# Kernel optimization log

Measured on AMD Instinct MI355X. Metric: run time of the kernel, lower is better.

Reference implementation:

```python
import jax, jax.numpy as jnp
import numpy as np

NEG = -9e15
ALPHA = 0.2  # leaky_relu negative slope


def setup_inputs() -> dict:
    key = jax.random.key(0)
    k1, k2, k3, k4, k5 = jax.random.split(key, 5)
    N, F_in, F_out = 8192, 128, 128
    x = jax.random.normal(k1, (N, F_in), dtype=jnp.float32)
    adj = jax.random.randint(k2, (N, N), 0, 2).astype(jnp.float32)
    # xavier-ish scaled params
    W = jax.random.normal(k3, (F_in, F_out), dtype=jnp.float32) * (1.0 / np.sqrt(F_in))
    a1 = jax.random.normal(k4, (F_out,), dtype=jnp.float32) * (1.0 / np.sqrt(2 * F_out))
    a2 = jax.random.normal(k5, (F_out,), dtype=jnp.float32) * (1.0 / np.sqrt(2 * F_out))
    a_bias = jnp.zeros((1,), dtype=jnp.float32)
    return {"x": x, "adj": adj, "W": W, "a1": a1, "a2": a2, "a_bias": a_bias}


def reference(x, adj, W, a1, a2, a_bias):
    # h = W(input)                                   [N, F]
    h = x @ W
    # a(concat(h_i, h_j)) == h_i.a1 + h_j.a2 + b  -> avoids N*N*2F concat
    s1 = h @ a1  # [N]
    s2 = h @ a2  # [N]
    e = jax.nn.leaky_relu(s1[:, None] + s2[None, :] + a_bias[0], negative_slope=ALPHA)  # [N, N]
    e = jnp.where(adj > 0, e, NEG)
    attention = jax.nn.softmax(e, axis=1)
    # dropout p=0 (deterministic eval): identity
    return attention @ h
```

## Files before the change

kernel.cpp:

```cpp
#include <hip/hip_runtime.h>
#include <hip/hip_bf16.h>

typedef __attribute__((ext_vector_type(8)))  __bf16         bf16x8;
typedef __attribute__((ext_vector_type(4)))  float          f32x4;
typedef __attribute__((ext_vector_type(8)))  unsigned short u16x8;

#define LOG2E 1.44269504088896340736f

#if __has_builtin(__builtin_amdgcn_exp2f)
#define EXP2F(x) __builtin_amdgcn_exp2f(x)
#else
#define EXP2F(x) __builtin_exp2f(x)
#endif

__device__ __forceinline__ unsigned short f2b(float f) {
  union { __bf16 h; unsigned short s; } o; o.h = (__bf16)f; return o.s;
}

__global__ __launch_bounds__(256) void k_prep(
    const float* __restrict__ x, const float* __restrict__ W,
    const float* __restrict__ a1, const float* __restrict__ a2,
    const float* __restrict__ ab,
    unsigned short* __restrict__ hT, float* __restrict__ s1p,
    float* __restrict__ s2p) {
  __shared__ __align__(16) float Ws[64 * 128];
  __shared__ __align__(16) float Xs[16 * 128];
  const int t = threadIdx.x;
  const int rb = blockIdx.x * 16;
  const int r  = t >> 4;
  const int fg = t & 15;

  {
    int off = t * 8;
    *(f32x4*)(Xs + off)     = *(const f32x4*)(x + (long)rb * 128 + off);
    *(f32x4*)(Xs + off + 4) = *(const f32x4*)(x + (long)rb * 128 + off + 4);
  }

  float acc[8];
#pragma unroll
  for (int j = 0; j < 8; ++j) acc[j] = 0.f;

  for (int half = 0; half < 2; ++half) {
    __syncthreads();
#pragma unroll
    for (int c = 0; c < 8; ++c) {
      int off = c * 1024 + t * 4;
      *(f32x4*)(Ws + off) = *(const f32x4*)(W + half * 8192 + off);
    }
    __syncthreads();
    for (int k = 0; k < 64; ++k) {
      float xv = Xs[r * 128 + half * 64 + k];
      f32x4 w0 = *(const f32x4*)(Ws + k * 128 + fg * 8);
      f32x4 w1 = *(const f32x4*)(Ws + k * 128 + fg * 8 + 4);
#pragma unroll
      for (int j = 0; j < 4; ++j) {
        acc[j]     += xv * w0[j];
        acc[4 + j] += xv * w1[j];
      }
    }
  }

  float p1 = 0.f, p2 = 0.f;
#pragma unroll
  for (int j = 0; j < 8; ++j) {
    p1 += acc[j] * a1[fg * 8 + j];
    p2 += acc[j] * a2[fg * 8 + j];
  }
#pragma unroll
  for (int mask = 1; mask <= 8; mask <<= 1) {
    p1 += __shfl_xor(p1, mask, 64);
    p2 += __shfl_xor(p2, mask, 64);
  }
  if (fg == 0) {
    s1p[rb + r] = LOG2E * (p1 + ab[0]);
    s2p[rb + r] = LOG2E * p2;
  }
#pragma unroll
  for (int j = 0; j < 8; ++j)
    hT[(long)(fg * 8 + j) * 8192 + rb + r] = f2b(acc[j]);
}

__global__ __launch_bounds__(512, 2) void k_attn(
    const float* __restrict__ adj, const unsigned short* __restrict__ hT,
    const float* __restrict__ s1p, const float* __restrict__ s2p,
    float* __restrict__ out) {
  __shared__ __align__(16) unsigned short Bs[128 * 128];
  __shared__ __align__(16) unsigned short As[32 * 136];
  __shared__ float dens[32];

  const int t = threadIdx.x;
  const int i0 = blockIdx.x * 32;
  const int lane = t & 63;
  const int wv = t >> 6;
  const int r  = t >> 4;
  const int kc = t & 15;
  const int m    = lane & 15;
  const int quad = lane >> 4;
  const int rt = wv & 1;
  const int f0 = (wv >> 1) * 32;

  const float s1v = s1p[i0 + r];
  const float* adjp = adj + (long)(i0 + r) * 8192 + kc * 8;
  const float* s2pp = s2p + kc * 8;

  f32x4 acc0, acc1;
#pragma unroll
  for (int p = 0; p < 4; ++p) { acc0[p] = 0.f; acc1[p] = 0.f; }
  float den = 0.f;

  f32x4 ar0 = __builtin_nontemporal_load((const f32x4*)(adjp));
  f32x4 ar1 = __builtin_nontemporal_load((const f32x4*)(adjp + 4));
  f32x4 cs0 = *(const f32x4*)(s2pp);
  f32x4 cs1 = *(const f32x4*)(s2pp + 4);
  u16x8 stg[4];
#pragma unroll
  for (int rr = 0; rr < 4; ++rr) {
    int f = rr * 32 + r;
    int cg = kc ^ (f & 7);
    stg[rr] = *(const u16x8*)(hT + (long)f * 8192 + cg * 8);
  }

  for (int it = 0; it < 64; ++it) {
#pragma unroll
    for (int rr = 0; rr < 4; ++rr) {
      int f = rr * 32 + r;
      *(u16x8*)(Bs + f * 128 + kc * 8) = stg[rr];
    }
    const int itn = (it + 1) & 63;
    f32x4 nr0 = __builtin_nontemporal_load((const f32x4*)(adjp + (long)itn * 128));
    f32x4 nr1 = __builtin_nontemporal_load((const f32x4*)(adjp + (long)itn * 128 + 4));
    f32x4 ns0 = *(const f32x4*)(s2pp + itn * 128);
    f32x4 ns1 = *(const f32x4*)(s2pp + itn * 128 + 4);

    u16x8 w;
    float dloc = 0.f;
#pragma unroll
    for (int j = 0; j < 4; ++j) {
      float tp = s1v + cs0[j];
      float wval = ar0[j] * EXP2F(fmaxf(tp, 0.2f * tp));
      dloc += wval; w[j] = f2b(wval);
    }
#pragma unroll
    for (int j = 0; j < 4; ++j) {
      float tp = s1v + cs1[j];
      float wval = ar1[j] * EXP2F(fmaxf(tp, 0.2f * tp));
      dloc += wval; w[4 + j] = f2b(wval);
    }
    den += dloc;
    *(u16x8*)(As + r * 136 + kc * 8) = w;

    __syncthreads();

    if (it < 63) {
      const unsigned short* hTi = hT + (long)(it + 1) * 128;
#pragma unroll
      for (int rr = 0; rr < 4; ++rr) {
        int f = rr * 32 + r;
        int cg = kc ^ (f & 7);
        stg[rr] = *(const u16x8*)(hTi + (long)f * 8192 + cg * 8);
      }
    }

#pragma unroll
    for (int ks = 0; ks < 4; ++ks) {
      bf16x8 af = *(const bf16x8*)(As + (rt * 16 + m) * 136 + ks * 32 + quad * 8);
      int c = ks * 4 + quad;
      {
        int f = f0 + m;
        int slot = c ^ (f & 7);
        bf16x8 bv = *(const bf16x8*)(Bs + f * 128 + slot * 8);
        acc0 = __builtin_amdgcn_mfma_f32_16x16x32_bf16(af, bv, acc0, 0, 0, 0);
      }
      {
        int f = f0 + 16 + m;
        int slot = c ^ (f & 7);
        bf16x8 bv = *(const bf16x8*)(Bs + f * 128 + slot * 8);
        acc1 = __builtin_amdgcn_mfma_f32_16x16x32_bf16(af, bv, acc1, 0, 0, 0);
      }
    }
    __syncthreads();

    ar0 = nr0; ar1 = nr1; cs0 = ns0; cs1 = ns1;
  }

  den += __shfl_xor(den, 1, 64);
  den += __shfl_xor(den, 2, 64);
  den += __shfl_xor(den, 4, 64);
  den += __shfl_xor(den, 8, 64);
  if (kc == 0) dens[r] = den;
  __syncthreads();

#pragma unroll
  for (int p = 0; p < 4; ++p) {
    int row = rt * 16 + quad * 4 + p;
    float d = dens[row];
    float inv = (d != 0.f) ? (1.f / d) : 0.f;
    out[(long)(i0 + row) * 128 + f0 + m]      = acc0[p] * inv;
    out[(long)(i0 + row) * 128 + f0 + 16 + m] = acc1[p] * inv;
  }
}

extern "C" void kernel_launch(void* const* d_in, const int* in_sizes, int n_in,
                              void* d_out, int out_size, void* d_ws, size_t ws_size,
                              hipStream_t stream) {
  int ix = 0, iadj = 1, iw = 2, ia1 = 3, ia2 = 4, iab = 5;
  {
    int f128[2] = {-1, -1};
    int tx = -1, tadj = -1, tw = -1, tab = -1, n128 = 0;
    for (int i = 0; i < n_in; ++i) {
      int s = in_sizes[i];
      if (s == 67108864) tadj = i;
      else if (s == 1048576) tx = i;
      else if (s == 16384) tw = i;
      else if (s == 128 && n128 < 2) f128[n128++] = i;
      else if (s == 1) tab = i;
    }
    if (tx >= 0 && tadj >= 0 && tw >= 0 && tab >= 0 && n128 == 2) {
      ix = tx; iadj = tadj; iw = tw; ia1 = f128[0]; ia2 = f128[1]; iab = tab;
    }
  }
  const float* x   = (const float*)d_in[ix];
  const float* adj = (const float*)d_in[iadj];
  const float* W   = (const float*)d_in[iw];
  const float* a1  = (const float*)d_in[ia1];
  const float* a2  = (const float*)d_in[ia2];
  const float* ab  = (const float*)d_in[iab];

  char* ws = (char*)d_ws;
  unsigned short* hT = (unsigned short*)(ws);
  float* s1p = (float*)(ws + 2097152);
  float* s2p = (float*)(ws + 2097152 + 32768);

  k_prep<<<dim3(512), dim3(256), 0, stream>>>(x, W, a1, a2, ab, hT, s1p, s2p);
  k_attn<<<dim3(256), dim3(512), 0, stream>>>(adj, hT, s1p, s2p, (float*)d_out);
}
```

Measured before the change: 389.0 us.

## Halve attention row tile to 16 rows and double grid size

The attention kernel now processes 16 query rows per block instead of 32 and launches 512 blocks, with each wave owning one 16-wide feature slice and one MFMA accumulator. Each thread loads four adjacency values per step instead of eight, and the launch bound asks for four blocks per CU. The aim is more blocks to fill the 256 CUs and more resident waves to hide adjacency streaming latency. In exchange, every block restages the full 128x128 hT tile each iteration for only half as many rows, which doubles hT L2 traffic and the LDS staging cost per unit of MFMA work.

Result: slower. 397.5 us (+2.2%).

```diff
diff --git a/kernel.cpp b/kernel.cpp
--- a/kernel.cpp
+++ b/kernel.cpp
@@ -80,74 +80,72 @@
     hT[(long)(fg * 8 + j) * 8192 + rb + r] = f2b(acc[j]);
 }
 
-__global__ __launch_bounds__(512, 2) void k_attn(
+__global__ __launch_bounds__(512, 4) void k_attn(
     const float* __restrict__ adj, const unsigned short* __restrict__ hT,
     const float* __restrict__ s1p, const float* __restrict__ s2p,
     float* __restrict__ out) {
   __shared__ __align__(16) unsigned short Bs[128 * 128];
-  __shared__ __align__(16) unsigned short As[32 * 136];
-  __shared__ float dens[32];
+  __shared__ __align__(16) unsigned short As[16 * 136];
+  __shared__ float dens[16];
 
   const int t = threadIdx.x;
-  const int i0 = blockIdx.x * 32;
+  const int i0 = blockIdx.x * 16;
   const int lane = t & 63;
   const int wv = t >> 6;
-  const int r  = t >> 4;
-  const int kc = t & 15;
   const int m    = lane & 15;
   const int quad = lane >> 4;
-  const int rt = wv & 1;
-  const int f0 = (wv >> 1) * 32;
-
-  const float s1v = s1p[i0 + r];
-  const float* adjp = adj + (long)(i0 + r) * 8192 + kc * 8;
-  const float* s2pp = s2p + kc * 8;
-
-  f32x4 acc0, acc1;
-#pragma unroll
-  for (int p = 0; p < 4; ++p) { acc0[p] = 0.f; acc1[p] = 0.f; }
+  const int f0 = wv * 16;
+
+  const int wr = t >> 5;
+  const int wc = t & 31;
+  const int sf    = t >> 4;
+  const int sslot = t & 15;
+
+  const float s1v = s1p[i0 + wr];
+  const float* adjp = adj + (long)(i0 + wr) * 8192 + wc * 4;
+  const float* s2pp = s2p + wc * 4;
+
+  f32x4 acc;
+#pragma unroll
+  for (int p = 0; p < 4; ++p) acc[p] = 0.f;
   float den = 0.f;
 
-  f32x4 ar0 = __builtin_nontemporal_load((const f32x4*)(adjp));
-  f32x4 ar1 = __builtin_nontemporal_load((const f32x4*)(adjp + 4));
-  f32x4 cs0 = *(const f32x4*)(s2pp);
-  f32x4 cs1 = *(const f32x4*)(s2pp + 4);
+  f32x4 ar = __builtin_nontemporal_load((const f32x4*)(adjp));
+  f32x4 cs = *(const f32x4*)(s2pp);
   u16x8 stg[4];
 #pragma unroll
   for (int rr = 0; rr < 4; ++rr) {
-    int f = rr * 32 + r;
-    int cg = kc ^ (f & 7);
+    int f = rr * 32 + sf;
+    int cg = sslot ^ (f & 7);
     stg[rr] = *(const u16x8*)(hT + (long)f * 8192 + cg * 8);
   }
 
   for (int it = 0; it < 64; ++it) {
 #pragma unroll
     for (int rr = 0; rr < 4; ++rr) {
-      int f = rr * 32 + r;
-      *(u16x8*)(Bs + f * 128 + kc * 8) = stg[rr];
+      int f = rr * 32 + sf;
+      *(u16x8*)(Bs + f * 128 + sslot * 8) = stg[rr];
     }
     const int itn = (it + 1) & 63;
-    f32x4 nr0 = __builtin_nontemporal_load((const f32x4*)(adjp + (long)itn * 128));
-    f32x4 nr1 = __builtin_nontemporal_load((const f32x4*)(adjp + (long)itn * 128 + 4));
-    f32x4 ns0 = *(const f32x4*)(s2pp + itn * 128);
-    f32x4 ns1 = *(const f32x4*)(s2pp + itn * 128 + 4);
-
-    u16x8 w;
-    float dloc = 0.f;
-#pragma unroll
-    for (int j = 0; j < 4; ++j) {
-      float tp = s1v + cs0[j];
-      float wval = ar0[j] * EXP2F(fmaxf(tp, 0.2f * tp));
-      dloc += wval; w[j] = f2b(wval);
-    }
-#pragma unroll
-    for (int j = 0; j < 4; ++j) {
-      float tp = s1v + cs1[j];
-      float wval = ar1[j] * EXP2F(fmaxf(tp, 0.2f * tp));
-      dloc += wval; w[4 + j] = f2b(wval);
-    }
-    den += dloc;
-    *(u16x8*)(As + r * 136 + kc * 8) = w;
+    f32x4 nr = __builtin_nontemporal_load((const f32x4*)(adjp + (long)itn * 128));
+    f32x4 ns = *(const f32x4*)(s2pp + itn * 128);
+
+    {
+      ushort4 w;
+      float dloc = 0.f;
+      float tp0 = s1v + cs[0];
+      float tp1 = s1v + cs[1];
+      float tp2 = s1v + cs[2];
+      float tp3 = s1v + cs[3];
+      float w0 = ar[0] * EXP2F(fmaxf(tp0, 0.2f * tp0));
+      float w1 = ar[1] * EXP2F(fmaxf(tp1, 0.2f * tp1));
+      float w2 = ar[2] * EXP2F(fmaxf(tp2, 0.2f * tp2));
+      float w3 = ar[3] * EXP2F(fmaxf(tp3, 0.2f * tp3));
+      dloc = (w0 + w1) + (w2 + w3);
+      w.x = f2b(w0); w.y = f2b(w1); w.z = f2b(w2); w.w = f2b(w3);
+      den += dloc;
+      *(ushort4*)(As + wr * 136 + wc * 4) = w;
+    }
 
     __syncthreads();
 
@@ -155,48 +153,38 @@
       const unsigned short* hTi = hT + (long)(it + 1) * 128;
 #pragma unroll
       for (int rr = 0; rr < 4; ++rr) {
-        int f = rr * 32 + r;
-        int cg = kc ^ (f & 7);
+        int f = rr * 32 + sf;
+        int cg = sslot ^ (f & 7);
         stg[rr] = *(const u16x8*)(hTi + (long)f * 8192 + cg * 8);
       }
     }
 
 #pragma unroll
     for (int ks = 0; ks < 4; ++ks) {
-      bf16x8 af = *(const bf16x8*)(As + (rt * 16 + m) * 136 + ks * 32 + quad * 8);
-      int c = ks * 4 + quad;
-      {
-        int f = f0 + m;
-        int slot = c ^ (f & 7);
-        bf16x8 bv = *(const bf16x8*)(Bs + f * 128 + slot * 8);
-        acc0 = __builtin_amdgcn_mfma_f32_16x16x32_bf16(af, bv, acc0, 0, 0, 0);
-      }
-      {
-        int f = f0 + 16 + m;
-        int slot = c ^ (f & 7);
-        bf16x8 bv = *(const bf16x8*)(Bs + f * 128 + slot * 8);
-        acc1 = __builtin_amdgcn_mfma_f32_16x16x32_bf16(af, bv, acc1, 0, 0, 0);
-      }
-    }
-    __syncthreads();
-
-    ar0 = nr0; ar1 = nr1; cs0 = ns0; cs1 = ns1;
+      bf16x8 af = *(const bf16x8*)(As + m * 136 + ks * 32 + quad * 8);
+      int slotx = (ks * 4 + quad) ^ ((f0 + m) & 7);
+      bf16x8 bv = *(const bf16x8*)(Bs + (f0 + m) * 128 + slotx * 8);
+      acc = __builtin_amdgcn_mfma_f32_16x16x32_bf16(af, bv, acc, 0, 0, 0);
+    }
+    __syncthreads();
+
+    ar = nr; cs = ns;
   }
 
   den += __shfl_xor(den, 1, 64);
   den += __shfl_xor(den, 2, 64);
   den += __shfl_xor(den, 4, 64);
   den += __shfl_xor(den, 8, 64);
-  if (kc == 0) dens[r] = den;
+  den += __shfl_xor(den, 16, 64);
+  if (wc == 0) dens[wr] = den;
   __syncthreads();
 
 #pragma unroll
   for (int p = 0; p < 4; ++p) {
-    int row = rt * 16 + quad * 4 + p;
+    int row = quad * 4 + p;
     float d = dens[row];
     float inv = (d != 0.f) ? (1.f / d) : 0.f;
-    out[(long)(i0 + row) * 128 + f0 + m]      = acc0[p] * inv;
-    out[(long)(i0 + row) * 128 + f0 + 16 + m] = acc1[p] * inv;
+    out[(long)(i0 + row) * 128 + f0 + m] = acc[p] * inv;
   }
 }
 
@@ -232,5 +220,5 @@
   float* s2p = (float*)(ws + 2097152 + 32768);
 
   k_prep<<<dim3(512), dim3(256), 0, stream>>>(x, W, a1, a2, ab, hT, s1p, s2p);
-  k_attn<<<dim3(256), dim3(512), 0, stream>>>(adj, hT, s1p, s2p, (float*)d_out);
-}
+  k_attn<<<dim3(512), dim3(512), 0, stream>>>(adj, hT, s1p, s2p, (float*)d_out);
+}
```
